# Performance work log

Measured on AMD Instinct MI355X. Metric: run time of the kernel, lower is better.

## Reference

```python
import jax, jax.numpy as jnp
import numpy as np

KERNEL_MUL = 2.0
KERNEL_NUM = 5
EPS = 1e-06


def setup_inputs() -> dict:
    key = jax.random.key(0)
    k1, k2 = jax.random.split(key)
    N, D = 4096, 256
    source = jax.random.normal(k1, (N, D), dtype=jnp.float32)
    target = jax.random.normal(k2, (N, D), dtype=jnp.float32)
    return {"source": source, "target": target}


def reference(source, target):
    n_src = source.shape[0]
    total = jnp.concatenate([source, target], axis=0)  # [2N, D]
    n = total.shape[0]
    # the broadcasted (total0 - total1)**2 sum, without the O(N^2*D) tensor).
    sq = jnp.sum(total * total, axis=1)  # [2N]
    L2 = sq[:, None] + sq[None, :] - 2.0 * (total @ total.T)  # [2N, 2N]
    # Bandwidth from detached distances (torch uses L2_distance.data).
    bandwidth = jax.lax.stop_gradient(jnp.sum(L2)) / (n * n - n)
    bandwidth = bandwidth / (KERNEL_MUL ** (KERNEL_NUM // 2))
    kernels = jnp.zeros_like(L2)
    for i in range(KERNEL_NUM):
        bw = bandwidth * (KERNEL_MUL ** i)
        kernels = kernels + jnp.exp(-L2 / (bw + EPS))
    XX = kernels[:n_src, :n_src]
    YY = kernels[n_src:, n_src:]
    XY = kernels[:n_src, n_src:]
    YX = kernels[n_src:, :n_src]
    return jnp.mean(XX + YY - XY - YX)
```

## Files before the change

kernel.cpp:

```cpp
#include <hip/hip_runtime.h>

#define N_TOT 8192
#define NS 4096
#define D 256
#define NB 64
#define NTRI (NB*(NB+1)/2)
#define HALF_B 32

typedef float f32x16 __attribute__((ext_vector_type(16)));
typedef float f32x2 __attribute__((ext_vector_type(2)));
typedef int i32x4 __attribute__((ext_vector_type(4)));
typedef int i32x8 __attribute__((ext_vector_type(8)));

__device__ __forceinline__ void gload16(const void* g, void* l) {
  __builtin_amdgcn_global_load_lds(
      (const __attribute__((address_space(1))) unsigned int*)g,
      (__attribute__((address_space(3))) unsigned int*)l,
      16, 0, 0);
}

__global__ void k_prep(const float* __restrict__ src, const float* __restrict__ tgt,
                       unsigned char* __restrict__ Xb, float* __restrict__ sqv,
                       float* __restrict__ pm, float* __restrict__ wsqp) {
  __shared__ float colacc[256];
  __shared__ float wred[4];
  int t = threadIdx.x, l = t & 63, w = t >> 6;
  colacc[t] = 0.f;
  __syncthreads();
  int base = blockIdx.x * 32;
  float c0 = 0.f, c1 = 0.f, c2 = 0.f, c3 = 0.f;
  float wsq = 0.f;
  #pragma unroll
  for (int r = 0; r < 8; ++r) {
    int row = base + w * 8 + r;
    const float* p = (row < NS) ? (src + (size_t)row * D) : (tgt + (size_t)(row - NS) * D);
    float4 v = ((const float4*)p)[l];
    int pk = __builtin_amdgcn_cvt_pk_fp8_f32(v.x, v.y, 0, false);
    pk = __builtin_amdgcn_cvt_pk_fp8_f32(v.z, v.w, pk, true);
    ((int*)(Xb + (size_t)row * D))[l] = pk;
    c0 += v.x; c1 += v.y; c2 += v.z; c3 += v.w;
    float s = fmaf(v.x, v.x, fmaf(v.y, v.y, fmaf(v.z, v.z, v.w * v.w)));
    for (int o = 32; o > 0; o >>= 1) s += __shfl_down(s, o, 64);
    if (l == 0) { sqv[row] = s; wsq += s; }
  }
  atomicAdd(&colacc[4 * l + 0], c0);
  atomicAdd(&colacc[4 * l + 1], c1);
  atomicAdd(&colacc[4 * l + 2], c2);
  atomicAdd(&colacc[4 * l + 3], c3);
  if (l == 0) wred[w] = wsq;
  __syncthreads();
  pm[blockIdx.x * 256 + t] = colacc[t];
  if (t == 0) wsqp[blockIdx.x] = (wred[0] + wred[1]) + (wred[2] + wred[3]);
}

__global__ __launch_bounds__(1024) void k_bw(const float* __restrict__ pm,
                                             const float* __restrict__ wsqp,
                                             float* __restrict__ coef) {
  __shared__ float csh[1024];
  __shared__ double red[256];
  int t = threadIdx.x;
  int col = t & 255, q = t >> 8;
  float cs = 0.f;
  #pragma unroll
  for (int b = 0; b < 64; ++b) cs += pm[(q * 64 + b) * 256 + col];
  csh[t] = cs;
  __syncthreads();
  if (t < 256) {
    float c = (csh[t] + csh[t + 256]) + (csh[t + 512] + csh[t + 768]);
    red[t] = (double)c * (double)c;
  }
  __syncthreads();
  for (int s = 128; s > 0; s >>= 1) {
    if (t < s) red[t] += red[t + s];
    __syncthreads();
  }
  double msq = red[0];
  __syncthreads();
  if (t < 256) red[t] = (double)wsqp[t];
  __syncthreads();
  for (int s = 128; s > 0; s >>= 1) {
    if (t < s) red[t] += red[t + s];
    __syncthreads();
  }
  if (t == 0) {
    double Sv = red[0];
    double n = (double)N_TOT;
    double sumL2 = 2.0 * n * Sv - 2.0 * msq;
    double bw = sumL2 / (n * n - n) / 4.0;
    double c4 = 1.0 / (bw * 16.0 + 1e-6);
    coef[0] = (float)(c4 * 1.4426950408889634);
  }
}

__global__ __launch_bounds__(256) void k_main(
    const unsigned char* __restrict__ Xb, const float* __restrict__ sqv,
    const float* __restrict__ coef, float* __restrict__ bpart) {
  int b = blockIdx.x;
  int bi = (int)((2.f * NB + 1.f - sqrtf((float)((2 * NB + 1) * (2 * NB + 1) - 8 * b))) * 0.5f);
  if (bi < 0) bi = 0;
  if (bi > NB - 1) bi = NB - 1;
  while ((bi + 1) * (2 * NB - bi) / 2 <= b) ++bi;
  while (bi * (2 * NB - bi + 1) / 2 > b) --bi;
  int bj = bi + (b - bi * (2 * NB - bi + 1) / 2);

  __shared__ unsigned char ldsA[128 * 64];
  __shared__ unsigned char ldsB[128 * 64];
  __shared__ float sqA[128], sqB[128];
  __shared__ float redw[4];

  int t = threadIdx.x, l = t & 63, w = t >> 6;
  int lr = l & 31, half = l >> 5;
  int waveRow = w >> 1, waveCol = w & 1;

  if (t < 128) sqA[t] = sqv[bi * 128 + t];
  else         sqB[t - 128] = sqv[bj * 128 + (t - 128)];
  float A4 = coef[0];

  const unsigned char* arow = Xb + (size_t)bi * 128 * D;
  const unsigned char* brow = Xb + (size_t)bj * 128 * D;

  f32x16 acc[2][2] = {};
  int cLo = 2 * half, cHi = 2 * half + 1;

  for (int ko = 0; ko < 4; ++ko) {
    if (ko) __syncthreads();
    int kOff = ko * 64;
    #pragma unroll
    for (int p = 0; p < 2; ++p) {
      int seg = p * 256 + t;
      int row = seg >> 2;
      int kb = (seg & 3) ^ (row & 3) ^ ((row >> 2) & 3);
      int goff = row * D + kOff + kb * 16;
      gload16(arow + goff, &ldsA[(p * 256 + w * 64) * 16]);
      gload16(brow + goff, &ldsB[(p * 256 + w * 64) * 16]);
    }
    __syncthreads();
    i32x8 aF[2];
    #pragma unroll
    for (int rb = 0; rb < 2; ++rb) {
      int rowA = waveRow * 64 + rb * 32 + lr;
      int sw = (rowA & 3) ^ ((rowA >> 2) & 3);
      i32x4 lo = *(const i32x4*)&ldsA[rowA * 64 + (cLo ^ sw) * 16];
      i32x4 hi = *(const i32x4*)&ldsA[rowA * 64 + (cHi ^ sw) * 16];
      aF[rb] = (i32x8){lo.x, lo.y, lo.z, lo.w, hi.x, hi.y, hi.z, hi.w};
    }
    #pragma unroll
    for (int cb = 0; cb < 2; ++cb) {
      int rowB = waveCol * 64 + cb * 32 + lr;
      int sw = (rowB & 3) ^ ((rowB >> 2) & 3);
      i32x4 lo = *(const i32x4*)&ldsB[rowB * 64 + (cLo ^ sw) * 16];
      i32x4 hi = *(const i32x4*)&ldsB[rowB * 64 + (cHi ^ sw) * 16];
      i32x8 bF = (i32x8){lo.x, lo.y, lo.z, lo.w, hi.x, hi.y, hi.z, hi.w};
      #pragma unroll
      for (int rb = 0; rb < 2; ++rb)
        acc[rb][cb] = __builtin_amdgcn_mfma_scale_f32_32x32x64_f8f6f4(
            aF[rb], bF, acc[rb][cb], 0, 0, 0, 127, 0, 127);
    }
  }

  float c2A4 = 2.f * A4, nA4 = -A4;
  f32x2 lsum2 = {0.f, 0.f};
  bool diag = (bi == bj);
  #pragma unroll
  for (int cb = 0; cb < 2; ++cb) {
    int jj = waveCol * 64 + cb * 32 + lr;
    float bjv = nA4 * sqB[jj];
    #pragma unroll
    for (int rb = 0; rb < 2; ++rb) {
      #pragma unroll
      for (int r = 0; r < 16; r += 2) {
        int ii = waveRow * 64 + rb * 32 + (r & 3) + 8 * (r >> 2) + 4 * half;
        f32x2 dot2 = {acc[rb][cb][r], acc[rb][cb][r + 1]};
        f32x2 sq2 = {sqA[ii], sqA[ii + 1]};
        f32x2 tt = c2A4 * dot2 + (nA4 * sq2 + bjv);
        f32x2 e;
        e.x = __builtin_amdgcn_exp2f(tt.x);
        e.y = __builtin_amdgcn_exp2f(tt.y);
        f32x2 e2 = e * e, e4 = e2 * e2, e8 = e4 * e4, e16 = e8 * e8;
        f32x2 kern = ((e + e2) + (e4 + e8)) + e16;
        if (diag) {
          if (ii == jj) kern.x = 0.f;
          if (ii + 1 == jj) kern.y = 0.f;
        }
        lsum2 += kern;
      }
    }
  }
  float lsum = lsum2.x + lsum2.y;
  for (int o = 32; o > 0; o >>= 1) lsum += __shfl_down(lsum, o, 64);
  if (l == 0) redw[w] = lsum;
  __syncthreads();
  if (t == 0) {
    float tot = (redw[0] + redw[1]) + (redw[2] + redw[3]);
    float wgt = diag ? 1.f : 2.f;
    float sgn = ((bi < HALF_B) == (bj < HALF_B)) ? 1.f : -1.f;
    bpart[b] = tot * wgt * sgn;
  }
}

__global__ void k_final(const float* __restrict__ bpart, float* __restrict__ out) {
  __shared__ double red[256];
  int t = threadIdx.x;
  double s = 0.0;
  #pragma unroll
  for (int k = 0; k < 9; ++k) {
    int idx = k * 256 + t;
    if (idx < NTRI) s += (double)bpart[idx];
  }
  red[t] = s;
  __syncthreads();
  for (int st = 128; st > 0; st >>= 1) {
    if (t < st) red[t] += red[t + st];
    __syncthreads();
  }
  if (t == 0) {
    double total = red[0] + 5.0 * (double)N_TOT;
    out[0] = (float)(total / ((double)NS * (double)NS));
  }
}

extern "C" void kernel_launch(void* const* d_in, const int* in_sizes, int n_in,
                              void* d_out, int out_size, void* d_ws, size_t ws_size,
                              hipStream_t stream) {
  const float* src = (const float*)d_in[0];
  const float* tgt = (const float*)d_in[1];
  float* out = (float*)d_out;
  char* ws = (char*)d_ws;
  unsigned char* Xb = (unsigned char*)ws;
  float* sqv  = (float*)(ws + (4u << 20));
  float* pm   = (float*)(ws + (4u << 20) + (32u << 10));
  float* wsqp = (float*)(ws + (4u << 20) + (288u << 10));
  float* coef = (float*)(ws + (4u << 20) + (289u << 10));
  float* bpart = (float*)(ws + (4u << 20) + (290u << 10));

  hipLaunchKernelGGL(k_prep, dim3(256), dim3(256), 0, stream, src, tgt, Xb, sqv, pm, wsqp);
  hipLaunchKernelGGL(k_bw, dim3(1), dim3(1024), 0, stream, pm, wsqp, coef);
  hipLaunchKernelGGL(k_main, dim3(NTRI), dim3(256), 0, stream, Xb, sqv, coef, bpart);
  hipLaunchKernelGGL(k_final, dim3(1), dim3(256), 0, stream, bpart, out);
}
```

Measured before the change: 94.91 us.

## Enlarge tiles to 256x256 with 16-wave blocks and double-buffered LDS staging

The main kernel now computes 256x256 triangular tiles using 1024-thread blocks (16 waves in a 4x4 grid), halving the tile count per dimension. Global-to-LDS loads are double-buffered with explicit vmcnt waits and raw barriers so the next K slice streams in while MFMAs run. Block indices are also permuted across a stride of 8 to spread work. This cuts redundant tile reloads and per-block overhead. The cost is fewer blocks (528), which weakens load balance across CUs and makes the diagonal tiles coarser.

Result: slower. 100.2 us (+5.6%).

```diff
diff --git a/kernel.cpp b/kernel.cpp
--- a/kernel.cpp
+++ b/kernel.cpp
@@ -3,9 +3,9 @@
 #define N_TOT 8192
 #define NS 4096
 #define D 256
-#define NB 64
-#define NTRI (NB*(NB+1)/2)
-#define HALF_B 32
+#define NB2 32
+#define NTRI2 (NB2*(NB2+1)/2)
+#define HALF_B2 16
 
 typedef float f32x16 __attribute__((ext_vector_type(16)));
 typedef float f32x2 __attribute__((ext_vector_type(2)));
@@ -92,69 +92,82 @@
   }
 }
 
-__global__ __launch_bounds__(256) void k_main(
+__global__ __launch_bounds__(1024, 4) void k_main(
     const unsigned char* __restrict__ Xb, const float* __restrict__ sqv,
     const float* __restrict__ coef, float* __restrict__ bpart) {
-  int b = blockIdx.x;
-  int bi = (int)((2.f * NB + 1.f - sqrtf((float)((2 * NB + 1) * (2 * NB + 1) - 8 * b))) * 0.5f);
+  int wg = (int)blockIdx.x;
+  int b = (wg % 8) * (NTRI2 / 8) + wg / 8;
+  int bi = (int)((2.f * NB2 + 1.f - sqrtf((float)((2 * NB2 + 1) * (2 * NB2 + 1) - 8 * b))) * 0.5f);
   if (bi < 0) bi = 0;
-  if (bi > NB - 1) bi = NB - 1;
-  while ((bi + 1) * (2 * NB - bi) / 2 <= b) ++bi;
-  while (bi * (2 * NB - bi + 1) / 2 > b) --bi;
-  int bj = bi + (b - bi * (2 * NB - bi + 1) / 2);
-
-  __shared__ unsigned char ldsA[128 * 64];
-  __shared__ unsigned char ldsB[128 * 64];
-  __shared__ float sqA[128], sqB[128];
-  __shared__ float redw[4];
+  if (bi > NB2 - 1) bi = NB2 - 1;
+  while ((bi + 1) * (2 * NB2 - bi) / 2 <= b) ++bi;
+  while (bi * (2 * NB2 - bi + 1) / 2 > b) --bi;
+  int bj = bi + (b - bi * (2 * NB2 - bi + 1) / 2);
+
+  __shared__ __align__(16) unsigned char ldsA[2][256 * 64];
+  __shared__ __align__(16) unsigned char ldsB[2][256 * 64];
+  __shared__ float sqA[256], sqB[256];
+  __shared__ float redw[16];
 
   int t = threadIdx.x, l = t & 63, w = t >> 6;
   int lr = l & 31, half = l >> 5;
-  int waveRow = w >> 1, waveCol = w & 1;
-
-  if (t < 128) sqA[t] = sqv[bi * 128 + t];
-  else         sqB[t - 128] = sqv[bj * 128 + (t - 128)];
+  int waveRow = w >> 2, waveCol = w & 3;
+
+  const unsigned char* arow = Xb + (size_t)bi * 256 * D;
+  const unsigned char* brow = Xb + (size_t)bj * 256 * D;
+
+  if (t < 256)      sqA[t] = sqv[bi * 256 + t];
+  else if (t < 512) sqB[t - 256] = sqv[bj * 256 + (t - 256)];
   float A4 = coef[0];
-
-  const unsigned char* arow = Xb + (size_t)bi * 128 * D;
-  const unsigned char* brow = Xb + (size_t)bj * 128 * D;
+  asm volatile("" :: "s"(A4));
+  asm volatile("" ::: "memory");
+
+  auto STAGE = [&](int k) {
+    int row = t >> 2;
+    int kb = (t & 3) ^ (row & 3) ^ ((row >> 2) & 3);
+    int goff = row * D + k * 64 + kb * 16;
+    gload16(arow + goff, &ldsA[k & 1][w * 1024]);
+    gload16(brow + goff, &ldsB[k & 1][w * 1024]);
+  };
+
+  STAGE(0);
+  STAGE(1);
 
   f32x16 acc[2][2] = {};
   int cLo = 2 * half, cHi = 2 * half + 1;
 
+  #pragma unroll
   for (int ko = 0; ko < 4; ++ko) {
-    if (ko) __syncthreads();
-    int kOff = ko * 64;
-    #pragma unroll
-    for (int p = 0; p < 2; ++p) {
-      int seg = p * 256 + t;
-      int row = seg >> 2;
-      int kb = (seg & 3) ^ (row & 3) ^ ((row >> 2) & 3);
-      int goff = row * D + kOff + kb * 16;
-      gload16(arow + goff, &ldsA[(p * 256 + w * 64) * 16]);
-      gload16(brow + goff, &ldsB[(p * 256 + w * 64) * 16]);
-    }
-    __syncthreads();
+    if (ko < 3)      asm volatile("s_waitcnt vmcnt(2)" ::: "memory");
+    else             asm volatile("s_waitcnt vmcnt(0)" ::: "memory");
+    __builtin_amdgcn_s_barrier();
+    const unsigned char* lA = &ldsA[ko & 1][0];
+    const unsigned char* lB = &ldsB[ko & 1][0];
     i32x8 aF[2];
     #pragma unroll
     for (int rb = 0; rb < 2; ++rb) {
       int rowA = waveRow * 64 + rb * 32 + lr;
       int sw = (rowA & 3) ^ ((rowA >> 2) & 3);
-      i32x4 lo = *(const i32x4*)&ldsA[rowA * 64 + (cLo ^ sw) * 16];
-      i32x4 hi = *(const i32x4*)&ldsA[rowA * 64 + (cHi ^ sw) * 16];
+      i32x4 lo = *(const i32x4*)&lA[rowA * 64 + (cLo ^ sw) * 16];
+      i32x4 hi = *(const i32x4*)&lA[rowA * 64 + (cHi ^ sw) * 16];
       aF[rb] = (i32x8){lo.x, lo.y, lo.z, lo.w, hi.x, hi.y, hi.z, hi.w};
     }
     #pragma unroll
     for (int cb = 0; cb < 2; ++cb) {
       int rowB = waveCol * 64 + cb * 32 + lr;
       int sw = (rowB & 3) ^ ((rowB >> 2) & 3);
-      i32x4 lo = *(const i32x4*)&ldsB[rowB * 64 + (cLo ^ sw) * 16];
-      i32x4 hi = *(const i32x4*)&ldsB[rowB * 64 + (cHi ^ sw) * 16];
+      i32x4 lo = *(const i32x4*)&lB[rowB * 64 + (cLo ^ sw) * 16];
+      i32x4 hi = *(const i32x4*)&lB[rowB * 64 + (cHi ^ sw) * 16];
       i32x8 bF = (i32x8){lo.x, lo.y, lo.z, lo.w, hi.x, hi.y, hi.z, hi.w};
       #pragma unroll
       for (int rb = 0; rb < 2; ++rb)
         acc[rb][cb] = __builtin_amdgcn_mfma_scale_f32_32x32x64_f8f6f4(
             aF[rb], bF, acc[rb][cb], 0, 0, 0, 127, 0, 127);
+    }
+    if (ko < 2) {
+      asm volatile("s_waitcnt lgkmcnt(0)" ::: "memory");
+      __builtin_amdgcn_s_barrier();
+      STAGE(ko + 2);
     }
   }
 
@@ -191,9 +204,11 @@
   if (l == 0) redw[w] = lsum;
   __syncthreads();
   if (t == 0) {
-    float tot = (redw[0] + redw[1]) + (redw[2] + redw[3]);
+    float tot = 0.f;
+    #pragma unroll
+    for (int i = 0; i < 16; ++i) tot += redw[i];
     float wgt = diag ? 1.f : 2.f;
-    float sgn = ((bi < HALF_B) == (bj < HALF_B)) ? 1.f : -1.f;
+    float sgn = ((bi < HALF_B2) == (bj < HALF_B2)) ? 1.f : -1.f;
     bpart[b] = tot * wgt * sgn;
   }
 }
@@ -203,9 +218,9 @@
   int t = threadIdx.x;
   double s = 0.0;
   #pragma unroll
-  for (int k = 0; k < 9; ++k) {
+  for (int k = 0; k < 3; ++k) {
     int idx = k * 256 + t;
-    if (idx < NTRI) s += (double)bpart[idx];
+    if (idx < NTRI2) s += (double)bpart[idx];
   }
   red[t] = s;
   __syncthreads();
@@ -235,6 +250,6 @@
 
   hipLaunchKernelGGL(k_prep, dim3(256), dim3(256), 0, stream, src, tgt, Xb, sqv, pm, wsqp);
   hipLaunchKernelGGL(k_bw, dim3(1), dim3(1024), 0, stream, pm, wsqp, coef);
-  hipLaunchKernelGGL(k_main, dim3(NTRI), dim3(256), 0, stream, Xb, sqv, coef, bpart);
+  hipLaunchKernelGGL(k_main, dim3(NTRI2), dim3(1024), 0, stream, Xb, sqv, coef, bpart);
   hipLaunchKernelGGL(k_final, dim3(1), dim3(256), 0, stream, bpart, out);
 }
```

## Store fp8 operands in MFMA fragment order and give each wave its own tile

Applied to the files above, without the earlier changes.

The prep kernel now writes the fp8 matrix in a pre-swizzled layout that matches the MFMA operand fragment order. This lets each wave load its A/B fragments straight from global memory with contiguous 32-byte reads, with no LDS staging and no block barriers. The main kernel switches from 128x128 block tiles shared by four waves to independent 64x64 wave tiles over a 128x128 triangular grid, with register double-buffered loads. Global/L2 traffic rises because operands are no longer reused across waves through LDS, and the final reduction now handles 8256 partials.

Result: no change. 96.50 us (+1.7%).

```diff
diff --git a/kernel.cpp b/kernel.cpp
--- a/kernel.cpp
+++ b/kernel.cpp
@@ -3,24 +3,17 @@
 #define N_TOT 8192
 #define NS 4096
 #define D 256
-#define NB 64
-#define NTRI (NB*(NB+1)/2)
-#define HALF_B 32
+#define NBW 128
+#define NTRIW (NBW*(NBW+1)/2)
+#define HALF_W 64
 
 typedef float f32x16 __attribute__((ext_vector_type(16)));
 typedef float f32x2 __attribute__((ext_vector_type(2)));
 typedef int i32x4 __attribute__((ext_vector_type(4)));
 typedef int i32x8 __attribute__((ext_vector_type(8)));
 
-__device__ __forceinline__ void gload16(const void* g, void* l) {
-  __builtin_amdgcn_global_load_lds(
-      (const __attribute__((address_space(1))) unsigned int*)g,
-      (__attribute__((address_space(3))) unsigned int*)l,
-      16, 0, 0);
-}
-
 __global__ void k_prep(const float* __restrict__ src, const float* __restrict__ tgt,
-                       unsigned char* __restrict__ Xb, float* __restrict__ sqv,
+                       unsigned char* __restrict__ Xf, float* __restrict__ sqv,
                        float* __restrict__ pm, float* __restrict__ wsqp) {
   __shared__ float colacc[256];
   __shared__ float wred[4];
@@ -30,6 +23,9 @@
   int base = blockIdx.x * 32;
   float c0 = 0.f, c1 = 0.f, c2 = 0.f, c3 = 0.f;
   float wsq = 0.f;
+  int ko = l >> 4;
+  int half = (l >> 3) & 1;
+  int off4 = l & 7;
   #pragma unroll
   for (int r = 0; r < 8; ++r) {
     int row = base + w * 8 + r;
@@ -37,7 +33,8 @@
     float4 v = ((const float4*)p)[l];
     int pk = __builtin_amdgcn_cvt_pk_fp8_f32(v.x, v.y, 0, false);
     pk = __builtin_amdgcn_cvt_pk_fp8_f32(v.z, v.w, pk, true);
-    ((int*)(Xb + (size_t)row * D))[l] = pk;
+    int g = row >> 5, rl = row & 31;
+    ((int*)Xf)[g * 2048 + ko * 512 + (half * 32 + rl) * 8 + off4] = pk;
     c0 += v.x; c1 += v.y; c2 += v.z; c3 += v.w;
     float s = fmaf(v.x, v.x, fmaf(v.y, v.y, fmaf(v.z, v.z, v.w * v.w)));
     for (int o = 32; o > 0; o >>= 1) s += __shfl_down(s, o, 64);
@@ -93,85 +90,71 @@
 }
 
 __global__ __launch_bounds__(256) void k_main(
-    const unsigned char* __restrict__ Xb, const float* __restrict__ sqv,
+    const unsigned char* __restrict__ Xf, const float* __restrict__ sqv,
     const float* __restrict__ coef, float* __restrict__ bpart) {
-  int b = blockIdx.x;
-  int bi = (int)((2.f * NB + 1.f - sqrtf((float)((2 * NB + 1) * (2 * NB + 1) - 8 * b))) * 0.5f);
-  if (bi < 0) bi = 0;
-  if (bi > NB - 1) bi = NB - 1;
-  while ((bi + 1) * (2 * NB - bi) / 2 <= b) ++bi;
-  while (bi * (2 * NB - bi + 1) / 2 > b) --bi;
-  int bj = bi + (b - bi * (2 * NB - bi + 1) / 2);
-
-  __shared__ unsigned char ldsA[128 * 64];
-  __shared__ unsigned char ldsB[128 * 64];
-  __shared__ float sqA[128], sqB[128];
-  __shared__ float redw[4];
-
   int t = threadIdx.x, l = t & 63, w = t >> 6;
   int lr = l & 31, half = l >> 5;
-  int waveRow = w >> 1, waveCol = w & 1;
-
-  if (t < 128) sqA[t] = sqv[bi * 128 + t];
-  else         sqB[t - 128] = sqv[bj * 128 + (t - 128)];
+  int b = blockIdx.x * 4 + w;
+  int bi = (int)((2.f * NBW + 1.f - sqrtf((float)((2 * NBW + 1) * (2 * NBW + 1) - 8 * b))) * 0.5f);
+  if (bi < 0) bi = 0;
+  if (bi > NBW - 1) bi = NBW - 1;
+  while ((bi + 1) * (2 * NBW - bi) / 2 <= b) ++bi;
+  while (bi * (2 * NBW - bi + 1) / 2 > b) --bi;
+  int bj = bi + (b - bi * (2 * NBW - bi + 1) / 2);
+
+  const unsigned char* pa = Xf + (size_t)(2 * bi) * 8192 + (size_t)l * 32;
+  const unsigned char* pb = Xf + (size_t)(2 * bj) * 8192 + (size_t)l * 32;
   float A4 = coef[0];
 
-  const unsigned char* arow = Xb + (size_t)bi * 128 * D;
-  const unsigned char* brow = Xb + (size_t)bj * 128 * D;
+  auto LD = [&](const unsigned char* base, int rb, int ko) -> i32x8 {
+    const unsigned char* p = base + rb * 8192 + ko * 2048;
+    i32x4 lo = *(const i32x4*)p;
+    i32x4 hi = *(const i32x4*)(p + 16);
+    return (i32x8){lo.x, lo.y, lo.z, lo.w, hi.x, hi.y, hi.z, hi.w};
+  };
+
+  i32x8 fa[2][2], fb[2][2];
+  #pragma unroll
+  for (int rb = 0; rb < 2; ++rb) {
+    fa[0][rb] = LD(pa, rb, 0); fb[0][rb] = LD(pb, rb, 0);
+    fa[1][rb] = LD(pa, rb, 1); fb[1][rb] = LD(pb, rb, 1);
+  }
 
   f32x16 acc[2][2] = {};
-  int cLo = 2 * half, cHi = 2 * half + 1;
-
+  #pragma unroll
   for (int ko = 0; ko < 4; ++ko) {
-    if (ko) __syncthreads();
-    int kOff = ko * 64;
+    const int cur = ko & 1;
     #pragma unroll
-    for (int p = 0; p < 2; ++p) {
-      int seg = p * 256 + t;
-      int row = seg >> 2;
-      int kb = (seg & 3) ^ (row & 3) ^ ((row >> 2) & 3);
-      int goff = row * D + kOff + kb * 16;
-      gload16(arow + goff, &ldsA[(p * 256 + w * 64) * 16]);
-      gload16(brow + goff, &ldsB[(p * 256 + w * 64) * 16]);
-    }
-    __syncthreads();
-    i32x8 aF[2];
-    #pragma unroll
-    for (int rb = 0; rb < 2; ++rb) {
-      int rowA = waveRow * 64 + rb * 32 + lr;
-      int sw = (rowA & 3) ^ ((rowA >> 2) & 3);
-      i32x4 lo = *(const i32x4*)&ldsA[rowA * 64 + (cLo ^ sw) * 16];
-      i32x4 hi = *(const i32x4*)&ldsA[rowA * 64 + (cHi ^ sw) * 16];
-      aF[rb] = (i32x8){lo.x, lo.y, lo.z, lo.w, hi.x, hi.y, hi.z, hi.w};
-    }
-    #pragma unroll
-    for (int cb = 0; cb < 2; ++cb) {
-      int rowB = waveCol * 64 + cb * 32 + lr;
-      int sw = (rowB & 3) ^ ((rowB >> 2) & 3);
-      i32x4 lo = *(const i32x4*)&ldsB[rowB * 64 + (cLo ^ sw) * 16];
-      i32x4 hi = *(const i32x4*)&ldsB[rowB * 64 + (cHi ^ sw) * 16];
-      i32x8 bF = (i32x8){lo.x, lo.y, lo.z, lo.w, hi.x, hi.y, hi.z, hi.w};
+    for (int cb = 0; cb < 2; ++cb)
       #pragma unroll
       for (int rb = 0; rb < 2; ++rb)
         acc[rb][cb] = __builtin_amdgcn_mfma_scale_f32_32x32x64_f8f6f4(
-            aF[rb], bF, acc[rb][cb], 0, 0, 0, 127, 0, 127);
+            fa[cur][rb], fb[cur][cb], acc[rb][cb], 0, 0, 0, 127, 0, 127);
+    if (ko < 2) {
+      #pragma unroll
+      for (int rb = 0; rb < 2; ++rb) {
+        fa[cur][rb] = LD(pa, rb, ko + 2);
+        fb[cur][rb] = LD(pb, rb, ko + 2);
+      }
     }
   }
 
+  const float* sqa = sqv + bi * 64;
+  const float* sqb = sqv + bj * 64;
   float c2A4 = 2.f * A4, nA4 = -A4;
   f32x2 lsum2 = {0.f, 0.f};
   bool diag = (bi == bj);
   #pragma unroll
   for (int cb = 0; cb < 2; ++cb) {
-    int jj = waveCol * 64 + cb * 32 + lr;
-    float bjv = nA4 * sqB[jj];
+    int jj = cb * 32 + lr;
+    float bjv = nA4 * sqb[jj];
     #pragma unroll
     for (int rb = 0; rb < 2; ++rb) {
       #pragma unroll
       for (int r = 0; r < 16; r += 2) {
-        int ii = waveRow * 64 + rb * 32 + (r & 3) + 8 * (r >> 2) + 4 * half;
+        int ii = rb * 32 + (r & 3) + 8 * (r >> 2) + 4 * half;
         f32x2 dot2 = {acc[rb][cb][r], acc[rb][cb][r + 1]};
-        f32x2 sq2 = {sqA[ii], sqA[ii + 1]};
+        f32x2 sq2 = *(const f32x2*)(sqa + ii);
         f32x2 tt = c2A4 * dot2 + (nA4 * sq2 + bjv);
         f32x2 e;
         e.x = __builtin_amdgcn_exp2f(tt.x);
@@ -188,13 +171,10 @@
   }
   float lsum = lsum2.x + lsum2.y;
   for (int o = 32; o > 0; o >>= 1) lsum += __shfl_down(lsum, o, 64);
-  if (l == 0) redw[w] = lsum;
-  __syncthreads();
-  if (t == 0) {
-    float tot = (redw[0] + redw[1]) + (redw[2] + redw[3]);
+  if (l == 0) {
     float wgt = diag ? 1.f : 2.f;
-    float sgn = ((bi < HALF_B) == (bj < HALF_B)) ? 1.f : -1.f;
-    bpart[b] = tot * wgt * sgn;
+    float sgn = ((bi < HALF_W) == (bj < HALF_W)) ? 1.f : -1.f;
+    bpart[b] = lsum * wgt * sgn;
   }
 }
 
@@ -203,9 +183,9 @@
   int t = threadIdx.x;
   double s = 0.0;
   #pragma unroll
-  for (int k = 0; k < 9; ++k) {
+  for (int k = 0; k < 33; ++k) {
     int idx = k * 256 + t;
-    if (idx < NTRI) s += (double)bpart[idx];
+    if (idx < NTRIW) s += (double)bpart[idx];
   }
   red[t] = s;
   __syncthreads();
@@ -226,15 +206,15 @@
   const float* tgt = (const float*)d_in[1];
   float* out = (float*)d_out;
   char* ws = (char*)d_ws;
-  unsigned char* Xb = (unsigned char*)ws;
+  unsigned char* Xf = (unsigned char*)ws;
   float* sqv  = (float*)(ws + (4u << 20));
   float* pm   = (float*)(ws + (4u << 20) + (32u << 10));
   float* wsqp = (float*)(ws + (4u << 20) + (288u << 10));
   float* coef = (float*)(ws + (4u << 20) + (289u << 10));
   float* bpart = (float*)(ws + (4u << 20) + (290u << 10));
 
-  hipLaunchKernelGGL(k_prep, dim3(256), dim3(256), 0, stream, src, tgt, Xb, sqv, pm, wsqp);
+  hipLaunchKernelGGL(k_prep, dim3(256), dim3(256), 0, stream, src, tgt, Xf, sqv, pm, wsqp);
   hipLaunchKernelGGL(k_bw, dim3(1), dim3(1024), 0, stream, pm, wsqp, coef);
-  hipLaunchKernelGGL(k_main, dim3(NTRI), dim3(256), 0, stream, Xb, sqv, coef, bpart);
+  hipLaunchKernelGGL(k_main, dim3(NTRIW / 4), dim3(256), 0, stream, Xf, sqv, coef, bpart);
   hipLaunchKernelGGL(k_final, dim3(1), dim3(256), 0, stream, bpart, out);
 }
```
